# Kernel optimization log

Measured on AMD Instinct MI355X. Metric: run time of the kernel, lower is better.

## Reference

```python
import jax, jax.numpy as jnp
import numpy as np

FILTER = [1.0, 3.0, 3.0, 1.0]
RADIUS = len(FILTER) // 2  # 2
UP = 2

def _make_kernel():
    # CreateLowpassKernel(Filter, Inplace=False): convolve with [1,1], outer product, normalize
    k1 = np.convolve(FILTER, [1.0, 1.0]).reshape(1, -1)  # [1,4,6,4,1]
    k = k1.T @ k1  # 5x5
    return jnp.asarray(k / k.sum(), dtype=jnp.float32)

def setup_inputs() -> dict:
    key = jax.random.key(0)
    x = jax.random.normal(key, (16, 128, 128, 128), dtype=jnp.float32)
    return {"x": x, "kernel": _make_kernel()}

def reference(x, kernel):
    # 1) reflect pad by FilterRadius on each spatial side
    r = RADIUS
    B, C, H, W = x.shape
    xp = jnp.pad(x, ((0, 0), (0, 0), (r, r), (r, r)), mode='reflect')
    # 2) upfirdn2d.upsample2d(xp, kernel, up=2, padding=-2r):
    #    zero-insert upsample by 2, pad0=(kw+up-1)//2-2r, pad1=(kw-up)//2-2r,
    #    convolve with flipped kernel scaled by gain=up**2=4.
    kh, kw = kernel.shape  # 5,5
    f = jnp.flip(kernel) * float(UP * UP)  # symmetric kernel, flip is a no-op but kept for fidelity
    p0 = (kw + UP - 1) // 2 - 2 * r       # = -1 (crop)
    p1 = (kw - UP) // 2 - 2 * r           # = -3 on the 2H grid
    # lax lhs_dilation produces size 2H'-1 (no trailing zero), so end pad is p1+1
    w = jnp.broadcast_to(f[None, None], (C, 1, kh, kw))
    y = jax.lax.conv_general_dilated(
        xp, w,
        window_strides=(1, 1),
        padding=[(p0, p1 + 1), (p0, p1 + 1)],
        lhs_dilation=(UP, UP),
        dimension_numbers=('NCHW', 'OIHW', 'NCHW'),
        feature_group_count=C)
    # y: [B, C, 2H, 2W]
    return y
```

## Files before the change

### kernel.cpp

```cpp
#include <hip/hip_runtime.h>


constexpr int H = 128, W = 128, OH = 256, OW = 256;
constexpr int TX  = 32;
constexpr int BY  = 8;
constexpr int YPT = 8;

typedef float f32x4 __attribute__((ext_vector_type(4)));

__global__ __launch_bounds__(256)
void up2x_kernel(const float* __restrict__ x, float* __restrict__ out) {
    const int tx    = threadIdx.x;
    const int ybase = (blockIdx.y * BY + threadIdx.y) * YPT;
    const int plane = blockIdx.z;

    const float* __restrict__ xin = x + (size_t)plane * (H * W);
    float* __restrict__ o = out + (size_t)plane * (OH * OW);

    float A[6], B[6], C[6];

    auto load_row = [&](const float* __restrict__ row, float* d) {
        const f32x4 v = *reinterpret_cast<const f32x4*>(row + 4 * tx);
        const float lft = __shfl(v.w, tx - 1, TX);
        const float rgt = __shfl(v.x, tx + 1, TX);
        d[0] = (tx == 0)      ? v.y : lft;
        d[1] = v.x; d[2] = v.y; d[3] = v.z; d[4] = v.w;
        d[5] = (tx == TX - 1) ? v.z : rgt;
    };

    load_row(xin + ((ybase == 0) ? 1 : ybase - 1) * W, A);
    load_row(xin + ybase * W, B);

    #pragma unroll
    for (int t = 0; t < YPT; ++t) {
        const int jy = ybase + t;
        load_row(xin + ((jy == H - 1) ? H - 2 : jy + 1) * W, C);

        float E[6], Q[6];
        #pragma unroll
        for (int c = 0; c < 6; ++c) {
            E[c] = 0.5f   * (A[c] + B[c]);
            Q[c] = 0.125f * (A[c] + 6.0f * B[c] + C[c]);
        }

        float to[8], bo[8];
        #pragma unroll
        for (int i = 0; i < 4; ++i) {
            to[2*i]   = 0.5f   * (E[i] + E[i+1]);
            to[2*i+1] = 0.125f * (E[i] + 6.0f * E[i+1] + E[i+2]);
            bo[2*i]   = 0.5f   * (Q[i] + Q[i+1]);
            bo[2*i+1] = 0.125f * (Q[i] + 6.0f * Q[i+1] + Q[i+2]);
        }

        float* r0 = o + (size_t)(2 * jy) * OW + 8 * tx;
        float* r1 = r0 + OW;
        f32x4 s0 = {to[0], to[1], to[2], to[3]};
        f32x4 s1 = {to[4], to[5], to[6], to[7]};
        f32x4 s2 = {bo[0], bo[1], bo[2], bo[3]};
        f32x4 s3 = {bo[4], bo[5], bo[6], bo[7]};
        __builtin_nontemporal_store(s0, reinterpret_cast<f32x4*>(r0));
        __builtin_nontemporal_store(s1, reinterpret_cast<f32x4*>(r0 + 4));
        __builtin_nontemporal_store(s2, reinterpret_cast<f32x4*>(r1));
        __builtin_nontemporal_store(s3, reinterpret_cast<f32x4*>(r1 + 4));

        #pragma unroll
        for (int c = 0; c < 6; ++c) { A[c] = B[c]; B[c] = C[c]; }
    }
}

extern "C" void kernel_launch(void* const* d_in, const int* in_sizes, int n_in,
                              void* d_out, int out_size, void* d_ws, size_t ws_size,
                              hipStream_t stream) {
    const float* x = (const float*)d_in[0];
    float* out = (float*)d_out;
    const int planes = in_sizes[0] / (H * W);

    dim3 block(TX, BY, 1);
    dim3 grid(1, H / (BY * YPT), planes);
    up2x_kernel<<<grid, block, 0, stream>>>(x, out);
}
```

Measured before the change: 717.3 us.

## Map one row across a full 64-lane wave with two columns per lane

Each input row is now handled by a full 64-lane wavefront. Every lane loads a float2 and writes one float4 to each of the two output rows, where before a 32-lane group loaded float4 and wrote two float4 per output row. Rows per thread drop from 8 to 4 and threads per block in y from 8 to 4, so more blocks cover each plane. The aim is fully contiguous 1KB wave-wide stores and more parallelism, at the cost of smaller loads and more halo-shuffle and row overhead per output element.

New measurement: 601.7 us. 1.19x faster.

```diff
diff --git a/kernel.cpp b/kernel.cpp
--- a/kernel.cpp
+++ b/kernel.cpp
@@ -2,30 +2,31 @@
 
 
 constexpr int H = 128, W = 128, OH = 256, OW = 256;
-constexpr int TX  = 32;
-constexpr int BY  = 8;
-constexpr int YPT = 8;
+constexpr int TX  = 64;
+constexpr int BY  = 4;
+constexpr int YPT = 4;
 
 typedef float f32x4 __attribute__((ext_vector_type(4)));
 
 __global__ __launch_bounds__(256)
 void up2x_kernel(const float* __restrict__ x, float* __restrict__ out) {
-    const int tx    = threadIdx.x;
+    const int lane  = threadIdx.x;
     const int ybase = (blockIdx.y * BY + threadIdx.y) * YPT;
     const int plane = blockIdx.z;
 
     const float* __restrict__ xin = x + (size_t)plane * (H * W);
     float* __restrict__ o = out + (size_t)plane * (OH * OW);
 
-    float A[6], B[6], C[6];
+    float A[4], B[4], C[4];
 
     auto load_row = [&](const float* __restrict__ row, float* d) {
-        const f32x4 v = *reinterpret_cast<const f32x4*>(row + 4 * tx);
-        const float lft = __shfl(v.w, tx - 1, TX);
-        const float rgt = __shfl(v.x, tx + 1, TX);
-        d[0] = (tx == 0)      ? v.y : lft;
-        d[1] = v.x; d[2] = v.y; d[3] = v.z; d[4] = v.w;
-        d[5] = (tx == TX - 1) ? v.z : rgt;
+        const float2 v = *reinterpret_cast<const float2*>(row + 2 * lane);
+        const float lft = __shfl(v.y, lane - 1, TX);
+        const float rgt = __shfl(v.x, lane + 1, TX);
+        d[0] = (lane == 0)      ? v.y : lft;
+        d[1] = v.x;
+        d[2] = v.y;
+        d[3] = (lane == TX - 1) ? v.x : rgt;
     };
 
     load_row(xin + ((ybase == 0) ? 1 : ybase - 1) * W, A);
@@ -36,35 +37,29 @@
         const int jy = ybase + t;
         load_row(xin + ((jy == H - 1) ? H - 2 : jy + 1) * W, C);
 
-        float E[6], Q[6];
+        float E[4], Q[4];
         #pragma unroll
-        for (int c = 0; c < 6; ++c) {
+        for (int c = 0; c < 4; ++c) {
             E[c] = 0.5f   * (A[c] + B[c]);
             Q[c] = 0.125f * (A[c] + 6.0f * B[c] + C[c]);
         }
 
-        float to[8], bo[8];
-        #pragma unroll
-        for (int i = 0; i < 4; ++i) {
-            to[2*i]   = 0.5f   * (E[i] + E[i+1]);
-            to[2*i+1] = 0.125f * (E[i] + 6.0f * E[i+1] + E[i+2]);
-            bo[2*i]   = 0.5f   * (Q[i] + Q[i+1]);
-            bo[2*i+1] = 0.125f * (Q[i] + 6.0f * Q[i+1] + Q[i+2]);
-        }
+        f32x4 top, bot;
+        top.x = 0.5f   * (E[0] + E[1]);
+        top.y = 0.125f * (E[0] + 6.0f * E[1] + E[2]);
+        top.z = 0.5f   * (E[1] + E[2]);
+        top.w = 0.125f * (E[1] + 6.0f * E[2] + E[3]);
+        bot.x = 0.5f   * (Q[0] + Q[1]);
+        bot.y = 0.125f * (Q[0] + 6.0f * Q[1] + Q[2]);
+        bot.z = 0.5f   * (Q[1] + Q[2]);
+        bot.w = 0.125f * (Q[1] + 6.0f * Q[2] + Q[3]);
 
-        float* r0 = o + (size_t)(2 * jy) * OW + 8 * tx;
-        float* r1 = r0 + OW;
-        f32x4 s0 = {to[0], to[1], to[2], to[3]};
-        f32x4 s1 = {to[4], to[5], to[6], to[7]};
-        f32x4 s2 = {bo[0], bo[1], bo[2], bo[3]};
-        f32x4 s3 = {bo[4], bo[5], bo[6], bo[7]};
-        __builtin_nontemporal_store(s0, reinterpret_cast<f32x4*>(r0));
-        __builtin_nontemporal_store(s1, reinterpret_cast<f32x4*>(r0 + 4));
-        __builtin_nontemporal_store(s2, reinterpret_cast<f32x4*>(r1));
-        __builtin_nontemporal_store(s3, reinterpret_cast<f32x4*>(r1 + 4));
+        float* r0 = o + (size_t)(2 * jy) * OW + 4 * lane;
+        __builtin_nontemporal_store(top, reinterpret_cast<f32x4*>(r0));
+        __builtin_nontemporal_store(bot, reinterpret_cast<f32x4*>(r0 + OW));
 
         #pragma unroll
-        for (int c = 0; c < 6; ++c) { A[c] = B[c]; B[c] = C[c]; }
+        for (int c = 0; c < 4; ++c) { A[c] = B[c]; B[c] = C[c]; }
     }
 }
 
```
